# Optimization experiments

Hardware: AMD Instinct MI355X
Metric: run time of the kernel (lower is better)

## Reference

```python
import jax, jax.numpy as jnp
import numpy as np

# Config mirroring My_MLP(mlp_layers=2, isize=512, k=30, non_linearity='relu',
#                        mlp_act='relu', offset_list=[2048]*4)
SIZES = [2048, 2048, 2048, 2048]   # per-client subgraph sizes (offset_list)
N = sum(SIZES)                      # 8192 total nodes
D = 512                             # isize
K = 30 + 1                          # module uses self.k + 1


def setup_inputs() -> dict:
    key = jax.random.key(0)
    k1, k2, k3 = jax.random.split(key, 3)
    features = jax.random.normal(k1, (N, D), dtype=jnp.float32)
    # Diag layer weights: a learned diagonal (vector) per layer, init near 1.
    w0 = 1.0 + 0.1 * jax.random.normal(k2, (D,), dtype=jnp.float32)
    w1 = 1.0 + 0.1 * jax.random.normal(k3, (D,), dtype=jnp.float32)
    return {"features": features, "w0": w0, "w1": w1}


def reference(features, w0, w1):
    # internal_forward: Diag -> relu -> Diag (no act after last layer)
    h = jax.nn.relu(features * w0) * w1                 # [N, D]
    # F.normalize(dim=1, p=2)
    emb = h * jax.lax.rsqrt(jnp.sum(h * h, axis=1, keepdims=True) + 1e-24)
    sim = jnp.matmul(emb, emb.T)                        # [N, N]

    # cross_subgraph_topk: per row, keep top-(k+1) similarities among columns
    # belonging to a DIFFERENT client subgraph; zero everything else.
    seg = jnp.asarray(np.repeat(np.arange(len(SIZES)), SIZES))   # [N] int
    same = seg[:, None] == seg[None, :]                           # [N, N] bool
    masked = jnp.where(same, -jnp.inf, sim)
    vals, inds = jax.lax.top_k(masked, K)                         # [N, K]
    rows = jnp.arange(N)[:, None]
    out = jnp.zeros_like(sim).at[rows, inds].set(vals)

    # apply_non_linearity('relu', i)
    return jax.nn.relu(out)
```

## Files before the change

kernel.cpp:

```cpp
#include <hip/hip_runtime.h>
#include <hip/hip_bf16.h>
#include <hip/hip_fp16.h>
#include <math.h>

typedef unsigned short u16;
typedef unsigned int u32;
typedef unsigned long long u64;
typedef __attribute__((ext_vector_type(8))) short bf16x8;
typedef __attribute__((ext_vector_type(4))) float f32x4;

#define N_NODES 8192
#define DIM 512
#define KSEL 31
#define BANDCAP 128
#define SEG_SIZE 2048
#define NVALID 6144
#define BAND_ULP 8

#define FENCE() asm volatile("s_waitcnt lgkmcnt(0)" ::: "memory")

__device__ __forceinline__ u32 f16key(u32 h) {
  return (h & 0x8000u) ? (0xFFFFu & ~h) : (h | 0x8000u);
}
__device__ __forceinline__ float keyval(u32 k) {
  const u16 raw = (k & 0x8000u) ? (u16)(k ^ 0x8000u) : (u16)(~k & 0xFFFFu);
  __half_raw hr; hr.x = raw;
  return __half2float(__half(hr));
}

#define GLD_LDS16(g, l)                                        \
  __builtin_amdgcn_global_load_lds(                            \
      (const __attribute__((address_space(1))) void*)(g),      \
      (__attribute__((address_space(3))) void*)(l), 16, 0, 0)

__global__ __launch_bounds__(256) void prep_kernel(
    const float* __restrict__ feat, const float* __restrict__ w0,
    const float* __restrict__ w1, u16* __restrict__ embh,
    float* __restrict__ embf, u32* __restrict__ kmax32) {
#pragma clang fp contract(off)
  const int row = blockIdx.x;
  const int t = threadIdx.x;
  __shared__ float hs[DIM];
  __shared__ float partial[32];
  __shared__ float rinv_sh;

  const float2 x = *reinterpret_cast<const float2*>(feat + (size_t)row * DIM + t * 2);
  const float2 a = *reinterpret_cast<const float2*>(w0 + t * 2);
  const float2 b = *reinterpret_cast<const float2*>(w1 + t * 2);
  const float h0 = fmaxf(x.x * a.x, 0.0f) * b.x;
  const float h1 = fmaxf(x.y * a.y, 0.0f) * b.y;
  hs[t * 2] = h0;
  hs[t * 2 + 1] = h1;
  if (t == 0) kmax32[row] = 0u;
  __syncthreads();

  if (t < 32) {
    const int base = (t >> 3) * 128 + (t & 7);
    float v = hs[base];
    float acc = v * v;
    for (int i = 1; i < 16; ++i) {
      v = hs[base + 8 * i];
      const float vv = v * v;
      acc = acc + vv;
    }
    partial[t] = acc;
  }
  __syncthreads();
  if (t == 0) {
    float B[4];
    for (int blk = 0; blk < 4; ++blk) {
      const float* p = &partial[blk * 8];
      B[blk] = ((p[0] + p[1]) + (p[2] + p[3])) + ((p[4] + p[5]) + (p[6] + p[7]));
    }
    const float s = (B[0] + B[1]) + (B[2] + B[3]);
    const float sp = s + 1e-24f;
    const float qf = (float)sqrt((double)sp);
    rinv_sh = (float)(1.0 / (double)qf);
  }
  __syncthreads();
  const float rinv = rinv_sh;
  const float e0 = h0 * rinv;
  const float e1 = h1 * rinv;
  *reinterpret_cast<float2*>(embf + (size_t)row * DIM + t * 2) = make_float2(e0, e1);
  __hip_bfloat162 bb;
  bb.x = __float2bfloat16(e0);
  bb.y = __float2bfloat16(e1);
  *reinterpret_cast<__hip_bfloat162*>(embh + (size_t)row * DIM + t * 2) = bb;
}

__global__ __launch_bounds__(256) void gemm_kernel(const u16* __restrict__ embh,
                                                   __half* __restrict__ simh,
                                                   u32* __restrict__ kmax32) {
  __shared__ u16 As[128][64];
  __shared__ u16 Bs[128][64];
  const int tid = threadIdx.x;
  const int lane = tid & 63;
  const int wave = tid >> 6;
  const int wm = wave >> 1;
  const int wn = wave & 1;
  const int rowTile = blockIdx.y;
  const int segTileBase = (rowTile >> 4) << 4;
  const int cT = blockIdx.x;
  const int colTile = cT < segTileBase ? cT : cT + 16;
  const int row0 = rowTile * 128;
  const int col0 = colTile * 128;

  f32x4 acc[4][4] = {};

  for (int k0 = 0; k0 < DIM; k0 += 64) {
#pragma unroll
    for (int i = 0; i < 4; ++i) {
      const int flat = i * 256 + tid;
      const int r = flat >> 3;
      const int c = (flat & 7) * 8;
      GLD_LDS16(embh + (size_t)(row0 + r) * DIM + k0 + c, &As[r][c]);
      GLD_LDS16(embh + (size_t)(col0 + r) * DIM + k0 + c, &Bs[r][c]);
    }
    __syncthreads();
#pragma unroll
    for (int kk = 0; kk < 2; ++kk) {
      bf16x8 afr[4], bfr[4];
      const int koff = kk * 32 + (lane >> 4) * 8;
      const int rsel = lane & 15;
#pragma unroll
      for (int m = 0; m < 4; ++m)
        afr[m] = *reinterpret_cast<const bf16x8*>(&As[wm * 64 + m * 16 + rsel][koff]);
#pragma unroll
      for (int n = 0; n < 4; ++n)
        bfr[n] = *reinterpret_cast<const bf16x8*>(&Bs[wn * 64 + n * 16 + rsel][koff]);
#pragma unroll
      for (int m = 0; m < 4; ++m)
#pragma unroll
        for (int n = 0; n < 4; ++n)
          acc[m][n] = __builtin_amdgcn_mfma_f32_16x16x32_bf16(afr[m], bfr[n],
                                                              acc[m][n], 0, 0, 0);
    }
    __syncthreads();
  }
#pragma unroll
  for (int m = 0; m < 4; ++m)
#pragma unroll
    for (int n = 0; n < 4; ++n)
#pragma unroll
      for (int j = 0; j < 4; ++j) {
        const int r = row0 + wm * 64 + m * 16 + (lane >> 4) * 4 + j;
        const int pcol = cT * 128 + wn * 64 + n * 16 + (lane & 15);
        simh[(size_t)r * NVALID + pcol] = __float2half(acc[m][n][j]);
      }
#pragma unroll
  for (int m = 0; m < 4; ++m) {
#pragma unroll
    for (int j = 0; j < 4; ++j) {
      float vmax = fmaxf(fmaxf(acc[m][0][j], acc[m][1][j]),
                         fmaxf(acc[m][2][j], acc[m][3][j]));
#pragma unroll
      for (int off = 1; off < 16; off <<= 1)
        vmax = fmaxf(vmax, __shfl_xor(vmax, off, 64));
      if ((lane & 15) == 0) {
        const int r = row0 + wm * 64 + m * 16 + (lane >> 4) * 4 + j;
        const u32 b = __float_as_uint(vmax);
        const u32 kk = (b & 0x80000000u) ? ~b : (b | 0x80000000u);
        atomicMax(&kmax32[r], kk);
      }
    }
  }
}

__global__ __launch_bounds__(256, 6) void select_kernel(
    const __half* __restrict__ simh, const float* __restrict__ embf,
    const u32* __restrict__ kmax32, int2* __restrict__ compact) {
  const int lane = threadIdx.x & 63;
  const int wave = threadIdx.x >> 6;
  const int row = blockIdx.x * 4 + wave;

  __shared__ __align__(16) float er[4][DIM];
  __shared__ u32 hist[4][257];
  __shared__ int bcol[4][BANDCAP];
  __shared__ float bex[4][BANDCAP];
  __shared__ int outidx_s[4][KSEL];
  __shared__ float outval_s[4][KSEL];
  __shared__ int cnts[4][2];

  const int segBase = (row >> 11) << 11;
  const uint4* src = reinterpret_cast<const uint4*>(simh + (size_t)row * NVALID);

  {
    const float4* ef = reinterpret_cast<const float4*>(embf + (size_t)row * DIM);
    reinterpret_cast<float4*>(&er[wave][lane * 8])[0] = ef[lane * 2];
    reinterpret_cast<float4*>(&er[wave][lane * 8])[1] = ef[lane * 2 + 1];
  }
  if (lane == 0) { cnts[wave][0] = 0; cnts[wave][1] = 0; }
  if (lane < KSEL) { outidx_s[wave][lane] = segBase; outval_s[wave][lane] = 0.0f; }

  u32 kmax16;
  {
    const u32 kk = kmax32[row];
    const u32 fb = (kk & 0x80000000u) ? (kk ^ 0x80000000u) : ~kk;
    const __half h = __float2half(__uint_as_float(fb));
    kmax16 = f16key((u32)__half_as_ushort(h));
  }

  u32 base = (kmax16 > 511u) ? kmax16 - 511u : 0u;
  u32 winTop = kmax16;
  u32 shift = 2;
  u32 need = KSEL;
  int tier = 0;
  u32 binlo = 0, binhi = 0;
  for (int guard = 0; guard < 6; ++guard) {
#pragma unroll
    for (int z = 0; z < 4; ++z) hist[wave][lane * 4 + z] = 0;
    FENCE();
    for (int j = 0; j < 12; ++j) {
      const uint4 v = src[j * 64 + lane];
      const u32 ws[4] = {v.x, v.y, v.z, v.w};
#pragma unroll
      for (int e = 0; e < 8; ++e) {
        const u32 k = f16key((ws[e >> 1] >> (16 * (e & 1))) & 0xFFFFu);
        if (k >= base && k <= winTop)
          atomicAdd(&hist[wave][(k - base) >> shift], 1u);
      }
    }
    FENCE();
    const int x = lane * 4;
    const u32 b0 = hist[wave][x], b1 = hist[wave][x + 1];
    const u32 b2 = hist[wave][x + 2], b3 = hist[wave][x + 3];
    const u32 tot = b0 + b1 + b2 + b3;
    u32 inc = tot;
#pragma unroll
    for (int off = 1; off < 64; off <<= 1) {
      const u32 vv = (u32)__shfl_down((int)inc, off, 64);
      if (lane + off < 64) inc += vv;
    }
    const u32 exc = inc - tot;
    const u32 g3 = exc, g2 = g3 + b3, g1 = g2 + b2, g0 = g1 + b1;
    int sel = -1;
    u32 gsel = 0;
    if (g3 < need && g3 + b3 >= need) { sel = x + 3; gsel = g3; }
    else if (g2 < need && g2 + b2 >= need) { sel = x + 2; gsel = g2; }
    else if (g1 < need && g1 + b1 >= need) { sel = x + 1; gsel = g1; }
    else if (g0 < need && g0 + b0 >= need) { sel = x;     gsel = g0; }
    const u64 bal = __ballot(sel >= 0);
    if (bal == 0) {
      if (tier == 0) { base = (kmax16 > 8191u) ? kmax16 - 8191u : 0u; shift = 5; }
      else { base = 0u; shift = 8; }
      winTop = kmax16; need = KSEL; tier++;
      continue;
    }
    const int srcl = (int)(__ffsll((unsigned long long)bal) - 1);
    sel  = __shfl(sel, srcl, 64);
    gsel = (u32)__shfl((int)gsel, srcl, 64);
    binlo = base + ((u32)sel << shift);
    binhi = min(binlo + (1u << shift) - 1u, winTop);
    if (shift > 2) {
      base = binlo; winTop = binhi; shift = 0; need = need - gsel;
      continue;
    }
    break;
  }

  const u32 hiK = binhi + BAND_ULP;
  const u32 loK = (binlo >= BAND_ULP) ? binlo - BAND_ULP : 0u;

  for (int j = 0; j < 12; ++j) {
    const uint4 v = src[j * 64 + lane];
    const u32 ws[4] = {v.x, v.y, v.z, v.w};
#pragma unroll
    for (int e = 0; e < 8; ++e) {
      const u32 k = f16key((ws[e >> 1] >> (16 * (e & 1))) & 0xFFFFu);
      if (k > hiK) {
        const int slot = atomicAdd(&cnts[wave][1], 1);
        const int i = ((j * 64 + lane) << 3) + e;
        if (slot < KSEL) {
          outidx_s[wave][slot] = (i < segBase) ? i : i + SEG_SIZE;
          outval_s[wave][slot] = fmaxf(keyval(k), 0.0f);
        }
      } else if (k >= loK) {
        const int slot = atomicAdd(&cnts[wave][0], 1);
        const int i = ((j * 64 + lane) << 3) + e;
        if (slot < BANDCAP) bcol[wave][slot] = (i < segBase) ? i : i + SEG_SIZE;
      }
    }
  }
  FENCE();
  const int nH = min(cnts[wave][1], KSEL);
  const int slots = KSEL - nH;
  const int nB = min(cnts[wave][0], BANDCAP);

  if (lane < nB) {
#pragma clang fp contract(off)
    const float4* g4 =
        reinterpret_cast<const float4*>(embf + (size_t)bcol[wave][lane] * DIM);
    const float4* e4 = reinterpret_cast<const float4*>(&er[wave][0]);
    float acc = 0.0f;
    for (int k4 = 0; k4 < DIM / 4; ++k4) {
      const float4 a = e4[k4];
      const float4 b = g4[k4];
      acc = acc + a.x * b.x;
      acc = acc + a.y * b.y;
      acc = acc + a.z * b.z;
      acc = acc + a.w * b.w;
    }
    bex[wave][lane] = acc;
  }
  FENCE();

  if (lane < nB) {
    const float ev = bex[wave][lane];
    const int ec = bcol[wave][lane];
    int r = 0;
    for (int j = 0; j < nB; ++j) {
      const float oj = bex[wave][j];
      const int cj = bcol[wave][j];
      if (oj > ev || (oj == ev && cj < ec)) r++;
    }
    if (r < slots) {
      const int slot = atomicAdd(&cnts[wave][1], 1);
      if (slot < KSEL) { outidx_s[wave][slot] = ec; outval_s[wave][slot] = fmaxf(ev, 0.0f); }
    }
  }
  FENCE();
  if (lane < KSEL)
    compact[(size_t)row * KSEL + lane] =
        make_int2(outidx_s[wave][lane], __float_as_int(outval_s[wave][lane]));
}

__global__ __launch_bounds__(256) void write_kernel(
    const int2* __restrict__ compact, float* __restrict__ out) {
  const int row = blockIdx.x;
  const int t = threadIdx.x;
  __shared__ int sidx[KSEL];
  __shared__ float sval[KSEL];
  if (t < KSEL) {
    const int2 e = compact[(size_t)row * KSEL + t];
    sidx[t] = e.x;
    sval[t] = __int_as_float(e.y);
  }
  float* orow = out + (size_t)row * N_NODES;
  const float4 zero4 = make_float4(0.f, 0.f, 0.f, 0.f);
  __syncthreads();
#pragma unroll
  for (int i = 0; i < 8; ++i)
    reinterpret_cast<float4*>(orow)[i * 256 + t] = zero4;
  __syncthreads();
  if (t < KSEL) orow[sidx[t]] = sval[t];
}

extern "C" void kernel_launch(void* const* d_in, const int* in_sizes, int n_in,
                              void* d_out, int out_size, void* d_ws, size_t ws_size,
                              hipStream_t stream) {
  const float* feat = (const float*)d_in[0];
  const float* w0 = (const float*)d_in[1];
  const float* w1 = (const float*)d_in[2];
  float* out = (float*)d_out;

  u16* embh = (u16*)d_ws;
  float* embf = (float*)((char*)d_ws + (size_t)N_NODES * DIM * 2);
  u32* kmax32 = (u32*)((char*)d_ws + (size_t)24 * 1024 * 1024);
  int2* compact = (int2*)d_ws;
  __half* simh = (__half*)d_out;

  prep_kernel<<<N_NODES, 256, 0, stream>>>(feat, w0, w1, embh, embf, kmax32);
  dim3 grid(48, 64);
  gemm_kernel<<<grid, 256, 0, stream>>>(embh, simh, kmax32);
  select_kernel<<<N_NODES / 4, 256, 0, stream>>>(simh, embf, kmax32, compact);
  write_kernel<<<N_NODES, 256, 0, stream>>>(compact, out);
}
```

Before: 251.3 us.

## Process one row per block in select kernel with register-cached keys

The select kernel now gives each row a whole 256-thread block instead of one wave, with 4 waves sharing one histogram. Each thread loads its 24 fp16 similarities once into registers as pre-converted sort keys, so the repeated histogram and band passes no longer re-read global memory. The cost is extra __syncthreads barriers, a shared-memory handoff of scan results from wave 0, and contention among four waves' atomics on a single LDS histogram. The row embedding is now read straight from global memory rather than staged in LDS.

```diff
diff --git a/kernel.cpp b/kernel.cpp
--- a/kernel.cpp
+++ b/kernel.cpp
@@ -17,10 +17,11 @@
 #define NVALID 6144
 #define BAND_ULP 8
 
-#define FENCE() asm volatile("s_waitcnt lgkmcnt(0)" ::: "memory")
-
 __device__ __forceinline__ u32 f16key(u32 h) {
   return (h & 0x8000u) ? (0xFFFFu & ~h) : (h | 0x8000u);
+}
+__device__ __forceinline__ u32 packkeys(u32 w) {
+  return f16key(w & 0xFFFFu) | (f16key(w >> 16) << 16);
 }
 __device__ __forceinline__ float keyval(u32 k) {
   const u16 raw = (k & 0x8000u) ? (u16)(k ^ 0x8000u) : (u16)(~k & 0xFFFFu);
@@ -166,31 +167,41 @@
   }
 }
 
-__global__ __launch_bounds__(256, 6) void select_kernel(
+__global__ __launch_bounds__(256) void select_kernel(
     const __half* __restrict__ simh, const float* __restrict__ embf,
     const u32* __restrict__ kmax32, int2* __restrict__ compact) {
-  const int lane = threadIdx.x & 63;
-  const int wave = threadIdx.x >> 6;
-  const int row = blockIdx.x * 4 + wave;
-
-  __shared__ __align__(16) float er[4][DIM];
-  __shared__ u32 hist[4][257];
-  __shared__ int bcol[4][BANDCAP];
-  __shared__ float bex[4][BANDCAP];
-  __shared__ int outidx_s[4][KSEL];
-  __shared__ float outval_s[4][KSEL];
-  __shared__ int cnts[4][2];
+  const int row = blockIdx.x;
+  const int t = threadIdx.x;
+  const int lane = t & 63;
+  const int wave = t >> 6;
+
+  __shared__ u32 hist[257];
+  __shared__ int bcol[BANDCAP];
+  __shared__ float bex[BANDCAP];
+  __shared__ int outidx_s[KSEL];
+  __shared__ float outval_s[KSEL];
+  __shared__ int cnts[2];
+  __shared__ u32 sh_lo, sh_hi, sh_need;
+  __shared__ int sh_state;
 
   const int segBase = (row >> 11) << 11;
-  const uint4* src = reinterpret_cast<const uint4*>(simh + (size_t)row * NVALID);
-
+
+  u32 pk[12];
   {
-    const float4* ef = reinterpret_cast<const float4*>(embf + (size_t)row * DIM);
-    reinterpret_cast<float4*>(&er[wave][lane * 8])[0] = ef[lane * 2];
-    reinterpret_cast<float4*>(&er[wave][lane * 8])[1] = ef[lane * 2 + 1];
-  }
-  if (lane == 0) { cnts[wave][0] = 0; cnts[wave][1] = 0; }
-  if (lane < KSEL) { outidx_s[wave][lane] = segBase; outval_s[wave][lane] = 0.0f; }
+    const uint4* src = reinterpret_cast<const uint4*>(simh + (size_t)row * NVALID);
+    const uint4 a = src[t], b = src[256 + t], c = src[512 + t];
+    pk[0] = packkeys(a.x); pk[1] = packkeys(a.y);
+    pk[2] = packkeys(a.z); pk[3] = packkeys(a.w);
+    pk[4] = packkeys(b.x); pk[5] = packkeys(b.y);
+    pk[6] = packkeys(b.z); pk[7] = packkeys(b.w);
+    pk[8] = packkeys(c.x); pk[9] = packkeys(c.y);
+    pk[10] = packkeys(c.z); pk[11] = packkeys(c.w);
+  }
+#define KEY(v) ((pk[(v) >> 1] >> (((v) & 1) * 16)) & 0xFFFFu)
+#define COL(v) ((((((v) >> 3) * 256) + t) << 3) + ((v) & 7))
+
+  if (t < KSEL) { outidx_s[t] = segBase; outval_s[t] = 0.0f; }
+  if (t == 0) { cnts[0] = 0; cnts[1] = 0; }
 
   u32 kmax16;
   {
@@ -205,92 +216,92 @@
   u32 shift = 2;
   u32 need = KSEL;
   int tier = 0;
-  u32 binlo = 0, binhi = 0;
   for (int guard = 0; guard < 6; ++guard) {
-#pragma unroll
-    for (int z = 0; z < 4; ++z) hist[wave][lane * 4 + z] = 0;
-    FENCE();
-    for (int j = 0; j < 12; ++j) {
-      const uint4 v = src[j * 64 + lane];
-      const u32 ws[4] = {v.x, v.y, v.z, v.w};
-#pragma unroll
-      for (int e = 0; e < 8; ++e) {
-        const u32 k = f16key((ws[e >> 1] >> (16 * (e & 1))) & 0xFFFFu);
-        if (k >= base && k <= winTop)
-          atomicAdd(&hist[wave][(k - base) >> shift], 1u);
-      }
-    }
-    FENCE();
-    const int x = lane * 4;
-    const u32 b0 = hist[wave][x], b1 = hist[wave][x + 1];
-    const u32 b2 = hist[wave][x + 2], b3 = hist[wave][x + 3];
-    const u32 tot = b0 + b1 + b2 + b3;
-    u32 inc = tot;
-#pragma unroll
-    for (int off = 1; off < 64; off <<= 1) {
-      const u32 vv = (u32)__shfl_down((int)inc, off, 64);
-      if (lane + off < 64) inc += vv;
-    }
-    const u32 exc = inc - tot;
-    const u32 g3 = exc, g2 = g3 + b3, g1 = g2 + b2, g0 = g1 + b1;
-    int sel = -1;
-    u32 gsel = 0;
-    if (g3 < need && g3 + b3 >= need) { sel = x + 3; gsel = g3; }
-    else if (g2 < need && g2 + b2 >= need) { sel = x + 2; gsel = g2; }
-    else if (g1 < need && g1 + b1 >= need) { sel = x + 1; gsel = g1; }
-    else if (g0 < need && g0 + b0 >= need) { sel = x;     gsel = g0; }
-    const u64 bal = __ballot(sel >= 0);
-    if (bal == 0) {
-      if (tier == 0) { base = (kmax16 > 8191u) ? kmax16 - 8191u : 0u; shift = 5; }
+    hist[t] = 0;
+    if (t == 0) hist[256] = 0;
+    __syncthreads();
+#pragma unroll
+    for (int v = 0; v < 24; ++v) {
+      const u32 k = KEY(v);
+      if (k >= base && k <= winTop) atomicAdd(&hist[(k - base) >> shift], 1u);
+    }
+    __syncthreads();
+    if (wave == 0) {
+      const int x = lane * 4;
+      const u32 b0 = hist[x], b1 = hist[x + 1];
+      const u32 b2 = hist[x + 2], b3 = hist[x + 3];
+      const u32 tot = b0 + b1 + b2 + b3;
+      u32 inc = tot;
+#pragma unroll
+      for (int off = 1; off < 64; off <<= 1) {
+        const u32 vv = (u32)__shfl_down((int)inc, off, 64);
+        if (lane + off < 64) inc += vv;
+      }
+      const u32 exc = inc - tot;
+      const u32 g3 = exc, g2 = g3 + b3, g1 = g2 + b2, g0 = g1 + b1;
+      int sel = -1;
+      u32 gsel = 0;
+      if (g3 < need && g3 + b3 >= need) { sel = x + 3; gsel = g3; }
+      else if (g2 < need && g2 + b2 >= need) { sel = x + 2; gsel = g2; }
+      else if (g1 < need && g1 + b1 >= need) { sel = x + 1; gsel = g1; }
+      else if (g0 < need && g0 + b0 >= need) { sel = x;     gsel = g0; }
+      const u64 bal = __ballot(sel >= 0);
+      if (lane == 0 && bal == 0) sh_state = 0;
+      if (bal != 0) {
+        const int srcl = (int)(__ffsll((unsigned long long)bal) - 1);
+        sel  = __shfl(sel, srcl, 64);
+        gsel = (u32)__shfl((int)gsel, srcl, 64);
+        if (lane == 0) {
+          const u32 blo = base + ((u32)sel << shift);
+          const u32 bhi = min(blo + (1u << shift) - 1u, winTop);
+          sh_lo = blo; sh_hi = bhi; sh_need = need - gsel;
+          sh_state = (shift > 2) ? 1 : 2;
+        }
+      }
+    }
+    __syncthreads();
+    const int st = sh_state;
+    if (st == 2) break;
+    if (st == 1) {
+      base = sh_lo; winTop = sh_hi; shift = 0; need = sh_need;
+    } else {
+      ++tier;
+      if (tier == 1) { base = (kmax16 > 8191u) ? kmax16 - 8191u : 0u; shift = 5; }
       else { base = 0u; shift = 8; }
-      winTop = kmax16; need = KSEL; tier++;
-      continue;
-    }
-    const int srcl = (int)(__ffsll((unsigned long long)bal) - 1);
-    sel  = __shfl(sel, srcl, 64);
-    gsel = (u32)__shfl((int)gsel, srcl, 64);
-    binlo = base + ((u32)sel << shift);
-    binhi = min(binlo + (1u << shift) - 1u, winTop);
-    if (shift > 2) {
-      base = binlo; winTop = binhi; shift = 0; need = need - gsel;
-      continue;
-    }
-    break;
-  }
-
+      winTop = kmax16; need = KSEL;
+    }
+    __syncthreads();
+  }
+  const u32 binlo = sh_lo, binhi = sh_hi;
   const u32 hiK = binhi + BAND_ULP;
   const u32 loK = (binlo >= BAND_ULP) ? binlo - BAND_ULP : 0u;
 
-  for (int j = 0; j < 12; ++j) {
-    const uint4 v = src[j * 64 + lane];
-    const u32 ws[4] = {v.x, v.y, v.z, v.w};
-#pragma unroll
-    for (int e = 0; e < 8; ++e) {
-      const u32 k = f16key((ws[e >> 1] >> (16 * (e & 1))) & 0xFFFFu);
-      if (k > hiK) {
-        const int slot = atomicAdd(&cnts[wave][1], 1);
-        const int i = ((j * 64 + lane) << 3) + e;
-        if (slot < KSEL) {
-          outidx_s[wave][slot] = (i < segBase) ? i : i + SEG_SIZE;
-          outval_s[wave][slot] = fmaxf(keyval(k), 0.0f);
-        }
-      } else if (k >= loK) {
-        const int slot = atomicAdd(&cnts[wave][0], 1);
-        const int i = ((j * 64 + lane) << 3) + e;
-        if (slot < BANDCAP) bcol[wave][slot] = (i < segBase) ? i : i + SEG_SIZE;
-      }
-    }
-  }
-  FENCE();
-  const int nH = min(cnts[wave][1], KSEL);
+#pragma unroll
+  for (int v = 0; v < 24; ++v) {
+    const u32 k = KEY(v);
+    if (k > hiK) {
+      const int slot = atomicAdd(&cnts[1], 1);
+      const int i = COL(v);
+      if (slot < KSEL) {
+        outidx_s[slot] = (i < segBase) ? i : i + SEG_SIZE;
+        outval_s[slot] = fmaxf(keyval(k), 0.0f);
+      }
+    } else if (k >= loK) {
+      const int slot = atomicAdd(&cnts[0], 1);
+      const int i = COL(v);
+      if (slot < BANDCAP) bcol[slot] = (i < segBase) ? i : i + SEG_SIZE;
+    }
+  }
+  __syncthreads();
+  const int nH = min(cnts[1], KSEL);
   const int slots = KSEL - nH;
-  const int nB = min(cnts[wave][0], BANDCAP);
-
-  if (lane < nB) {
+  const int nB = min(cnts[0], BANDCAP);
+
+  if (t < nB) {
 #pragma clang fp contract(off)
     const float4* g4 =
-        reinterpret_cast<const float4*>(embf + (size_t)bcol[wave][lane] * DIM);
-    const float4* e4 = reinterpret_cast<const float4*>(&er[wave][0]);
+        reinterpret_cast<const float4*>(embf + (size_t)bcol[t] * DIM);
+    const float4* e4 = reinterpret_cast<const float4*>(embf + (size_t)row * DIM);
     float acc = 0.0f;
     for (int k4 = 0; k4 < DIM / 4; ++k4) {
       const float4 a = e4[k4];
@@ -300,28 +311,30 @@
       acc = acc + a.z * b.z;
       acc = acc + a.w * b.w;
     }
-    bex[wave][lane] = acc;
-  }
-  FENCE();
-
-  if (lane < nB) {
-    const float ev = bex[wave][lane];
-    const int ec = bcol[wave][lane];
+    bex[t] = acc;
+  }
+  __syncthreads();
+
+  if (t < nB) {
+    const float ev = bex[t];
+    const int ec = bcol[t];
     int r = 0;
     for (int j = 0; j < nB; ++j) {
-      const float oj = bex[wave][j];
-      const int cj = bcol[wave][j];
+      const float oj = bex[j];
+      const int cj = bcol[j];
       if (oj > ev || (oj == ev && cj < ec)) r++;
     }
     if (r < slots) {
-      const int slot = atomicAdd(&cnts[wave][1], 1);
-      if (slot < KSEL) { outidx_s[wave][slot] = ec; outval_s[wave][slot] = fmaxf(ev, 0.0f); }
-    }
-  }
-  FENCE();
-  if (lane < KSEL)
-    compact[(size_t)row * KSEL + lane] =
-        make_int2(outidx_s[wave][lane], __float_as_int(outval_s[wave][lane]));
+      const int slot = atomicAdd(&cnts[1], 1);
+      if (slot < KSEL) { outidx_s[slot] = ec; outval_s[slot] = fmaxf(ev, 0.0f); }
+    }
+  }
+  __syncthreads();
+  if (t < KSEL)
+    compact[(size_t)row * KSEL + t] =
+        make_int2(outidx_s[t], __float_as_int(outval_s[t]));
+#undef KEY
+#undef COL
 }
 
 __global__ __launch_bounds__(256) void write_kernel(
@@ -362,6 +375,6 @@
   prep_kernel<<<N_NODES, 256, 0, stream>>>(feat, w0, w1, embh, embf, kmax32);
   dim3 grid(48, 64);
   gemm_kernel<<<grid, 256, 0, stream>>>(embh, simh, kmax32);
-  select_kernel<<<N_NODES / 4, 256, 0, stream>>>(simh, embf, kmax32, compact);
+  select_kernel<<<N_NODES, 256, 0, stream>>>(simh, embf, kmax32, compact);
   write_kernel<<<N_NODES, 256, 0, stream>>>(compact, out);
 }
```

Result: faster. 246.3 us (-2.0%).
